# Performance work log

Hardware: AMD Instinct MI355X
Metric: run time of the kernel (lower is better)

The kernel has to match this reference:

```python
import jax, jax.numpy as jnp
import numpy as np

ALPHA = 0.1   # alpha_factor
BETA = 1.0    # beta_factor
NUM_CLASSES = 1000
B, D = 4096, 512


def setup_inputs() -> dict:
    key = jax.random.key(0)
    ks = jax.random.split(key, 7)
    return {
        "anchor": jax.random.normal(ks[0], (B, D), dtype=jnp.float32),
        "positive": jax.random.normal(ks[1], (B, D), dtype=jnp.float32),
        "negative": jax.random.normal(ks[2], (B, D), dtype=jnp.float32),
        "outputs": jax.random.normal(ks[3], (3 * B, NUM_CLASSES), dtype=jnp.float32),
        "labels_anchor": jax.random.randint(ks[4], (B,), 0, NUM_CLASSES, dtype=jnp.int32).astype(jnp.int64),
        "labels_neg": jax.random.randint(ks[5], (B,), 0, NUM_CLASSES, dtype=jnp.int32).astype(jnp.int64),
        "exemplars": jax.random.normal(ks[6], (NUM_CLASSES, D), dtype=jnp.float32),
    }


def reference(anchor, positive, negative, outputs, labels_anchor, labels_neg, exemplars):
    # cross-entropy (mean reduction) over concatenated labels [3B]
    labels = jnp.concatenate([labels_anchor, labels_anchor, labels_neg], axis=0)
    logp = jax.nn.log_softmax(outputs, axis=-1)                       # [3B, C]
    loss_softmax = -jnp.mean(jnp.take_along_axis(logp, labels[:, None], axis=1))

    # pairwise L2 distances anchor-to-exemplars via ||a||^2 + ||e||^2 - 2 a.e  -> [B, C]
    a_sq = jnp.sum(anchor * anchor, axis=1, keepdims=True)            # [B, 1]
    e_sq = jnp.sum(exemplars * exemplars, axis=1)[None, :]            # [1, C]
    d2 = a_sq + e_sq - 2.0 * (anchor @ exemplars.T)                   # [B, C]
    d_all = jnp.sqrt(jnp.maximum(d2, 0.0))

    d_ref = jnp.take_along_axis(d_all, labels_anchor[:, None], axis=1)[:, 0]  # [B]
    d_closest = jnp.min(d_all, axis=1)                                # [B]
    loss_center = jnp.sum(jax.nn.relu(d_ref - d_closest))

    tp = jnp.linalg.norm(anchor - positive, axis=1)                   # [B]
    tn = jnp.linalg.norm(anchor - negative, axis=1)                   # [B]
    loss_triplet = jnp.sum(jax.nn.relu(tp - tn))

    loss_total = loss_softmax + ALPHA * loss_center + BETA * loss_triplet
    return (loss_total, loss_triplet, loss_softmax, loss_center)
```

## Files before the change

### kernel.cpp

```cpp
#include <hip/hip_runtime.h>
#include <math.h>

#define BB 4096
#define DD 512
#define CC 1000

typedef __attribute__((ext_vector_type(8))) short short8;
typedef __attribute__((ext_vector_type(4))) float f32x4;

#define OFF_ABF  0
#define OFF_EBF  1048576
#define OFF_ESQ  1310720
#define OFF_ASQ  1311744
#define OFF_DREF 1315840
#define OFF_PMIN 1319936
#define OFF_CEP  1324032
#define OFF_TRP  1327104

__device__ __forceinline__ unsigned short f2bf(float x) {
    unsigned u = __float_as_uint(x);
    unsigned r = (u + 0x7FFFu + ((u >> 16) & 1u)) >> 16;
    return (unsigned short)r;
}

__global__ __launch_bounds__(256) void prep_kernel(
    const float* __restrict__ a, const float* __restrict__ p,
    const float* __restrict__ n, const float* __restrict__ ex,
    const int* __restrict__ la,
    unsigned short* __restrict__ Abf, unsigned short* __restrict__ Ebf,
    float* __restrict__ esq, float* __restrict__ asq,
    float* __restrict__ dref, float* __restrict__ tr_part,
    float* __restrict__ pmin)
{
    const int bid = blockIdx.x;
    const int wid = threadIdx.x >> 6, lane = threadIdx.x & 63;
    if (bid < 1024) {
        const int i = bid * 4 + wid;
        const int label = la[i];
        const float4* ar = (const float4*)(a + (size_t)i * DD);
        const float4* pr = (const float4*)(p + (size_t)i * DD);
        const float4* nr = (const float4*)(n + (size_t)i * DD);
        const float4* er = (const float4*)(ex + (size_t)label * DD);
        float sa = 0.f, sp = 0.f, sn = 0.f, se = 0.f;
#pragma unroll
        for (int k = 0; k < 2; k++) {
            const int j = lane + k * 64;
            float4 av = ar[j], pv = pr[j], nv = nr[j], ev = er[j];
            union { unsigned short u[4]; uint2 q; } o;
            o.u[0]=f2bf(av.x); o.u[1]=f2bf(av.y); o.u[2]=f2bf(av.z); o.u[3]=f2bf(av.w);
            *(uint2*)(Abf + (size_t)i * DD + j * 4) = o.q;
            sa += av.x*av.x + av.y*av.y + av.z*av.z + av.w*av.w;
            float dx = av.x-pv.x, dy = av.y-pv.y, dz = av.z-pv.z, dw = av.w-pv.w;
            sp += dx*dx + dy*dy + dz*dz + dw*dw;
            dx = av.x-nv.x; dy = av.y-nv.y; dz = av.z-nv.z; dw = av.w-nv.w;
            sn += dx*dx + dy*dy + dz*dz + dw*dw;
            dx = av.x-ev.x; dy = av.y-ev.y; dz = av.z-ev.z; dw = av.w-ev.w;
            se += dx*dx + dy*dy + dz*dz + dw*dw;
        }
        for (int off = 32; off; off >>= 1) {
            sa += __shfl_xor(sa, off);
            sp += __shfl_xor(sp, off);
            sn += __shfl_xor(sn, off);
            se += __shfl_xor(se, off);
        }
        __shared__ float ts[4];
        if (lane == 0) {
            asq[i]  = sa;
            dref[i] = sqrtf(se);
            pmin[i] = INFINITY;
            ts[wid] = fmaxf(sqrtf(sp) - sqrtf(sn), 0.f);
        }
        __syncthreads();
        if (threadIdx.x == 0) tr_part[bid] = ts[0] + ts[1] + ts[2] + ts[3];
    } else {
        const int c = (bid - 1024) * 4 + wid;
        float s = 0.f;
        if (c < CC) {
            const float4* row = (const float4*)(ex + (size_t)c * DD);
#pragma unroll
            for (int k = 0; k < 2; k++) {
                const int j = lane + k * 64;
                float4 v = row[j];
                union { unsigned short u[4]; uint2 q; } o;
                o.u[0]=f2bf(v.x); o.u[1]=f2bf(v.y); o.u[2]=f2bf(v.z); o.u[3]=f2bf(v.w);
                *(uint2*)(Ebf + (size_t)c * DD + j * 4) = o.q;
                s += v.x*v.x + v.y*v.y + v.z*v.z + v.w*v.w;
            }
            for (int off = 32; off; off >>= 1) s += __shfl_xor(s, off);
        } else {
            const uint2 z = make_uint2(0, 0);
#pragma unroll
            for (int k = 0; k < 2; k++) {
                const int j = lane + k * 64;
                *(uint2*)(Ebf + (size_t)c * DD + j * 4) = z;
            }
        }
        if (lane == 0) esq[c] = s;
    }
}

#define GL2LDS(gsrc, ldst) __builtin_amdgcn_global_load_lds( \
    (const __attribute__((address_space(1))) unsigned int*)(gsrc), \
    (__attribute__((address_space(3))) unsigned int*)(ldst), 16, 0, 0)

__global__ __launch_bounds__(512) void main_kernel(
    const unsigned short* __restrict__ Ab, const unsigned short* __restrict__ Eb,
    const float* __restrict__ asq, const float* __restrict__ esq,
    const float* __restrict__ outp,
    const int* __restrict__ la, const int* __restrict__ ln,
    float* __restrict__ pmin, float* __restrict__ ce_part)
{
    __shared__ unsigned short lA[2][256 * 32];
    __shared__ unsigned short lB[2][128 * 32];
    __shared__ float s_pm[2][256];
    __shared__ float ps[8];

    const int bid = blockIdx.x;
    const int tid = threadIdx.x;
    const int w = tid >> 6, lane = tid & 63;

    if (bid < 128) {
        const int wm = w >> 1, wn = w & 1;
        const int hi = lane >> 4, lo = lane & 15;
        const int gm0 = (bid >> 3) * 256, gn0 = (bid & 7) * 128;

        const int r0 = tid >> 2, q0 = tid & 3;
        const int sw0 = q0 ^ ((r0 >> 1) & 3);
        const size_t srcA0 = ((size_t)(gm0 + r0) << 9) + (sw0 << 3);
        const size_t srcA1 = ((size_t)(gm0 + 128 + r0) << 9) + (sw0 << 3);
        const size_t srcB  = ((size_t)(gn0 + r0) << 9) + (sw0 << 3);
        const int dstA = (w << 9);

#define STAGE(buf, kt) do { \
        GL2LDS(Ab + srcA0 + ((kt) << 5), &lA[buf][dstA]); \
        GL2LDS(Ab + srcA1 + ((kt) << 5), &lA[buf][4096 + dstA]); \
        GL2LDS(Eb + srcB  + ((kt) << 5), &lB[buf][dstA]); \
    } while (0)

        f32x4 acc[4][4];
#pragma unroll
        for (int mi = 0; mi < 4; mi++)
#pragma unroll
            for (int ni = 0; ni < 4; ni++) acc[mi][ni] = (f32x4){0.f, 0.f, 0.f, 0.f};

        STAGE(0, 0);
        for (int kt = 0; kt < 16; kt++) {
            const int buf = kt & 1;
            if (kt < 15) {
                STAGE(buf ^ 1, kt + 1);
                asm volatile("s_waitcnt vmcnt(3)" ::: "memory");
            } else {
                asm volatile("s_waitcnt vmcnt(0)" ::: "memory");
            }
            __builtin_amdgcn_s_barrier();
            asm volatile("" ::: "memory");

            short8 af[4], bf[4];
#pragma unroll
            for (int mi = 0; mi < 4; mi++) {
                int r = (wm << 6) + (mi << 4) + lo;
                af[mi] = *(const short8*)&lA[buf][(r << 5) + ((hi ^ ((r >> 1) & 3)) << 3)];
            }
#pragma unroll
            for (int ni = 0; ni < 4; ni++) {
                int r = (wn << 6) + (ni << 4) + lo;
                bf[ni] = *(const short8*)&lB[buf][(r << 5) + ((hi ^ ((r >> 1) & 3)) << 3)];
            }
#pragma unroll
            for (int mi = 0; mi < 4; mi++)
#pragma unroll
                for (int ni = 0; ni < 4; ni++)
                    acc[mi][ni] = __builtin_amdgcn_mfma_f32_16x16x32_bf16(af[mi], bf[ni], acc[mi][ni], 0, 0, 0);

            asm volatile("" ::: "memory");
            __builtin_amdgcn_s_barrier();
        }
#undef STAGE

        float aq[4][4];
#pragma unroll
        for (int mi = 0; mi < 4; mi++) {
            float4 a0 = *(const float4*)&asq[gm0 + wm * 64 + mi * 16 + hi * 4];
            aq[mi][0]=a0.x; aq[mi][1]=a0.y; aq[mi][2]=a0.z; aq[mi][3]=a0.w;
        }
        float esqc[4]; int bad[4];
#pragma unroll
        for (int ni = 0; ni < 4; ni++) {
            int gn = gn0 + wn * 64 + ni * 16 + lo;
            esqc[ni] = esq[gn];
            bad[ni] = (gn >= CC);
        }
        float vmin[4][4];
#pragma unroll
        for (int mi = 0; mi < 4; mi++)
#pragma unroll
            for (int j = 0; j < 4; j++) {
                float best = INFINITY;
#pragma unroll
                for (int ni = 0; ni < 4; ni++) {
                    float d2 = aq[mi][j] + esqc[ni] - 2.f * acc[mi][ni][j];
                    float d = sqrtf(fmaxf(d2, 0.f));
                    if (bad[ni]) d = INFINITY;
                    best = fminf(best, d);
                }
                vmin[mi][j] = best;
            }
#pragma unroll
        for (int off = 1; off < 16; off <<= 1)
#pragma unroll
            for (int mi = 0; mi < 4; mi++)
#pragma unroll
                for (int j = 0; j < 4; j++)
                    vmin[mi][j] = fminf(vmin[mi][j], __shfl_xor(vmin[mi][j], off));

        if (lo == 0) {
#pragma unroll
            for (int mi = 0; mi < 4; mi++)
#pragma unroll
                for (int j = 0; j < 4; j++)
                    s_pm[wn][wm * 64 + mi * 16 + hi * 4 + j] = vmin[mi][j];
        }
        __syncthreads();
        if (tid < 256) {
            float m2 = fminf(s_pm[0][tid], s_pm[1][tid]);
            atomicMin((int*)pmin + gm0 + tid, __float_as_int(m2));
        }
    } else {
        const int cb = bid - 128;
        const int r = cb * 8 + w;
        const int label = (r < 2 * BB) ? la[r & (BB - 1)] : ln[r - 2 * BB];
        const float4* row4 = (const float4*)(outp + (size_t)r * CC);
        float4 v[4];
#pragma unroll
        for (int k = 0; k < 4; k++) {
            int j4 = lane + k * 64;
            v[k] = (j4 < 250) ? row4[j4]
                              : make_float4(-INFINITY, -INFINITY, -INFINITY, -INFINITY);
        }
        float m = -INFINITY;
#pragma unroll
        for (int k = 0; k < 4; k++)
            m = fmaxf(m, fmaxf(fmaxf(v[k].x, v[k].y), fmaxf(v[k].z, v[k].w)));
        for (int off = 32; off; off >>= 1) m = fmaxf(m, __shfl_xor(m, off));

        const int lj4 = label >> 2, lc = label & 3;
        float s = 0.f, lv = 0.f;
#pragma unroll
        for (int k = 0; k < 4; k++) {
            int j4 = lane + k * 64;
            s += __expf(v[k].x - m) + __expf(v[k].y - m)
               + __expf(v[k].z - m) + __expf(v[k].w - m);
            float comp = (lc == 0) ? v[k].x : (lc == 1) ? v[k].y : (lc == 2) ? v[k].z : v[k].w;
            lv += (j4 == lj4) ? comp : 0.f;
        }
        for (int off = 32; off; off >>= 1) {
            s += __shfl_xor(s, off);
            lv += __shfl_xor(lv, off);
        }
        if (lane == 0) ps[w] = -(lv - m - __logf(s));
        __syncthreads();
        if (tid == 0) {
            float t = 0.f;
#pragma unroll
            for (int q = 0; q < 8; q++) t += ps[q];
            ce_part[cb] = t;
        }
    }
}

__global__ __launch_bounds__(1024) void final_kernel(
    const float* __restrict__ ce_part, const float* __restrict__ tr_part,
    const float* __restrict__ pmin, const float* __restrict__ dref,
    float* __restrict__ out)
{
    int tid = threadIdx.x;
    float ce = 0.f, tr = tr_part[tid], ctr = 0.f;
    if (tid < 1536) ce = ce_part[tid] + ((tid < 512) ? ce_part[tid + 1024] : 0.f);
#pragma unroll
    for (int a = 0; a < 4; a++) {
        int m = a * 1024 + tid;
        ctr += fmaxf(dref[m] - pmin[m], 0.f);
    }
    for (int off = 32; off; off >>= 1) {
        ce += __shfl_xor(ce, off);
        tr += __shfl_xor(tr, off);
        ctr += __shfl_xor(ctr, off);
    }
    __shared__ float s[3][16];
    int wid = tid >> 6, lane = tid & 63;
    if (lane == 0) { s[0][wid] = ce; s[1][wid] = tr; s[2][wid] = ctr; }
    __syncthreads();
    if (tid == 0) {
        float tce = 0.f, ttr = 0.f, tctr = 0.f;
#pragma unroll
        for (int w = 0; w < 16; w++) { tce += s[0][w]; ttr += s[1][w]; tctr += s[2][w]; }
        float lsm = tce / (3.f * BB);
        out[0] = lsm + 0.1f * tctr + 1.0f * ttr;
        out[1] = ttr;
        out[2] = lsm;
        out[3] = tctr;
    }
}

extern "C" void kernel_launch(void* const* d_in, const int* in_sizes, int n_in,
                              void* d_out, int out_size, void* d_ws, size_t ws_size,
                              hipStream_t stream) {
    const float* anchor   = (const float*)d_in[0];
    const float* positive = (const float*)d_in[1];
    const float* negative = (const float*)d_in[2];
    const float* outputs  = (const float*)d_in[3];
    const int*   la       = (const int*)d_in[4];
    const int*   ln       = (const int*)d_in[5];
    const float* ex       = (const float*)d_in[6];
    float* out = (float*)d_out;
    float* ws  = (float*)d_ws;

    unsigned short* Abf = (unsigned short*)(ws + OFF_ABF);
    unsigned short* Ebf = (unsigned short*)(ws + OFF_EBF);
    float* esq      = ws + OFF_ESQ;
    float* asq      = ws + OFF_ASQ;
    float* dref     = ws + OFF_DREF;
    float* pmin     = ws + OFF_PMIN;
    float* ce_part  = ws + OFF_CEP;
    float* tr_part  = ws + OFF_TRP;

    hipLaunchKernelGGL(prep_kernel,  dim3(1280), dim3(256),  0, stream,
                       anchor, positive, negative, ex, la, Abf, Ebf, esq, asq, dref, tr_part, pmin);
    hipLaunchKernelGGL(main_kernel,  dim3(1664), dim3(512),  0, stream,
                       Abf, Ebf, asq, esq, outputs, la, ln, pmin, ce_part);
    hipLaunchKernelGGL(final_kernel, dim3(1),    dim3(1024), 0, stream,
                       ce_part, tr_part, pmin, dref, out);
}
```

Baseline: 36.05 us.

## Move cross-entropy into prep kernel and run GEMM as its own small kernel

Moves the bandwidth-bound cross-entropy row processing out of the GEMM kernel and into the first kernel, alongside bf16 conversion and norm computation, using 512-thread blocks. The GEMM becomes a standalone 128-block kernel with a swapped tile index order (M-fastest). The aim is to overlap the large logits read with the prep work and to stop the GEMM blocks from sharing a launch with memory-bound CE blocks. The trade-off is that the GEMM now runs alone on only 128 blocks and can leave most CUs idle.

After: 38.08 us. 5.6% more time.

```diff
diff --git a/kernel.cpp b/kernel.cpp
--- a/kernel.cpp
+++ b/kernel.cpp
@@ -23,19 +23,62 @@
     return (unsigned short)r;
 }
 
-__global__ __launch_bounds__(256) void prep_kernel(
+__global__ __launch_bounds__(512) void k1_kernel(
     const float* __restrict__ a, const float* __restrict__ p,
     const float* __restrict__ n, const float* __restrict__ ex,
-    const int* __restrict__ la,
+    const float* __restrict__ outp,
+    const int* __restrict__ la, const int* __restrict__ ln,
     unsigned short* __restrict__ Abf, unsigned short* __restrict__ Ebf,
     float* __restrict__ esq, float* __restrict__ asq,
     float* __restrict__ dref, float* __restrict__ tr_part,
-    float* __restrict__ pmin)
+    float* __restrict__ pmin, float* __restrict__ ce_part)
 {
+    __shared__ float ps[8];
     const int bid = blockIdx.x;
-    const int wid = threadIdx.x >> 6, lane = threadIdx.x & 63;
-    if (bid < 1024) {
-        const int i = bid * 4 + wid;
+    const int tid = threadIdx.x;
+    const int w = tid >> 6, lane = tid & 63;
+
+    if (bid < 1536) {
+        const int r = bid * 8 + w;
+        const int label = (r < 2 * BB) ? la[r & (BB - 1)] : ln[r - 2 * BB];
+        const float4* row4 = (const float4*)(outp + (size_t)r * CC);
+        float4 v[4];
+#pragma unroll
+        for (int k = 0; k < 4; k++) {
+            int j4 = lane + k * 64;
+            v[k] = (j4 < 250) ? row4[j4]
+                              : make_float4(-INFINITY, -INFINITY, -INFINITY, -INFINITY);
+        }
+        float m = -INFINITY;
+#pragma unroll
+        for (int k = 0; k < 4; k++)
+            m = fmaxf(m, fmaxf(fmaxf(v[k].x, v[k].y), fmaxf(v[k].z, v[k].w)));
+        for (int off = 32; off; off >>= 1) m = fmaxf(m, __shfl_xor(m, off));
+
+        const int lj4 = label >> 2, lc = label & 3;
+        float s = 0.f, lv = 0.f;
+#pragma unroll
+        for (int k = 0; k < 4; k++) {
+            int j4 = lane + k * 64;
+            s += __expf(v[k].x - m) + __expf(v[k].y - m)
+               + __expf(v[k].z - m) + __expf(v[k].w - m);
+            float comp = (lc == 0) ? v[k].x : (lc == 1) ? v[k].y : (lc == 2) ? v[k].z : v[k].w;
+            lv += (j4 == lj4) ? comp : 0.f;
+        }
+        for (int off = 32; off; off >>= 1) {
+            s += __shfl_xor(s, off);
+            lv += __shfl_xor(lv, off);
+        }
+        if (lane == 0) ps[w] = -(lv - m - __logf(s));
+        __syncthreads();
+        if (tid == 0) {
+            float t = 0.f;
+#pragma unroll
+            for (int q = 0; q < 8; q++) t += ps[q];
+            ce_part[bid] = t;
+        }
+    } else if (bid < 2048) {
+        const int i = (bid - 1536) * 8 + w;
         const int label = la[i];
         const float4* ar = (const float4*)(a + (size_t)i * DD);
         const float4* pr = (const float4*)(p + (size_t)i * DD);
@@ -63,17 +106,21 @@
             sn += __shfl_xor(sn, off);
             se += __shfl_xor(se, off);
         }
-        __shared__ float ts[4];
         if (lane == 0) {
             asq[i]  = sa;
             dref[i] = sqrtf(se);
             pmin[i] = INFINITY;
-            ts[wid] = fmaxf(sqrtf(sp) - sqrtf(sn), 0.f);
+            ps[w] = fmaxf(sqrtf(sp) - sqrtf(sn), 0.f);
         }
         __syncthreads();
-        if (threadIdx.x == 0) tr_part[bid] = ts[0] + ts[1] + ts[2] + ts[3];
+        if (tid == 0) {
+            float t = 0.f;
+#pragma unroll
+            for (int q = 0; q < 8; q++) t += ps[q];
+            tr_part[bid - 1536] = t;
+        }
     } else {
-        const int c = (bid - 1024) * 4 + wid;
+        const int c = (bid - 2048) * 8 + w;
         float s = 0.f;
         if (c < CC) {
             const float4* row = (const float4*)(ex + (size_t)c * DD);
@@ -103,168 +150,123 @@
     (const __attribute__((address_space(1))) unsigned int*)(gsrc), \
     (__attribute__((address_space(3))) unsigned int*)(ldst), 16, 0, 0)
 
-__global__ __launch_bounds__(512) void main_kernel(
+__global__ __launch_bounds__(512) void gemm_kernel(
     const unsigned short* __restrict__ Ab, const unsigned short* __restrict__ Eb,
     const float* __restrict__ asq, const float* __restrict__ esq,
-    const float* __restrict__ outp,
-    const int* __restrict__ la, const int* __restrict__ ln,
-    float* __restrict__ pmin, float* __restrict__ ce_part)
+    float* __restrict__ pmin)
 {
     __shared__ unsigned short lA[2][256 * 32];
     __shared__ unsigned short lB[2][128 * 32];
     __shared__ float s_pm[2][256];
-    __shared__ float ps[8];
 
     const int bid = blockIdx.x;
     const int tid = threadIdx.x;
     const int w = tid >> 6, lane = tid & 63;
 
-    if (bid < 128) {
-        const int wm = w >> 1, wn = w & 1;
-        const int hi = lane >> 4, lo = lane & 15;
-        const int gm0 = (bid >> 3) * 256, gn0 = (bid & 7) * 128;
-
-        const int r0 = tid >> 2, q0 = tid & 3;
-        const int sw0 = q0 ^ ((r0 >> 1) & 3);
-        const size_t srcA0 = ((size_t)(gm0 + r0) << 9) + (sw0 << 3);
-        const size_t srcA1 = ((size_t)(gm0 + 128 + r0) << 9) + (sw0 << 3);
-        const size_t srcB  = ((size_t)(gn0 + r0) << 9) + (sw0 << 3);
-        const int dstA = (w << 9);
+    const int wm = w >> 1, wn = w & 1;
+    const int hi = lane >> 4, lo = lane & 15;
+    const int gm0 = (bid & 15) * 256, gn0 = (bid >> 4) * 128;
+
+    const int r0 = tid >> 2, q0 = tid & 3;
+    const int sw0 = q0 ^ ((r0 >> 1) & 3);
+    const size_t srcA0 = ((size_t)(gm0 + r0) << 9) + (sw0 << 3);
+    const size_t srcA1 = ((size_t)(gm0 + 128 + r0) << 9) + (sw0 << 3);
+    const size_t srcB  = ((size_t)(gn0 + r0) << 9) + (sw0 << 3);
+    const int dstA = (w << 9);
 
 #define STAGE(buf, kt) do { \
-        GL2LDS(Ab + srcA0 + ((kt) << 5), &lA[buf][dstA]); \
-        GL2LDS(Ab + srcA1 + ((kt) << 5), &lA[buf][4096 + dstA]); \
-        GL2LDS(Eb + srcB  + ((kt) << 5), &lB[buf][dstA]); \
-    } while (0)
-
-        f32x4 acc[4][4];
+    GL2LDS(Ab + srcA0 + ((kt) << 5), &lA[buf][dstA]); \
+    GL2LDS(Ab + srcA1 + ((kt) << 5), &lA[buf][4096 + dstA]); \
+    GL2LDS(Eb + srcB  + ((kt) << 5), &lB[buf][dstA]); \
+} while (0)
+
+    f32x4 acc[4][4];
+#pragma unroll
+    for (int mi = 0; mi < 4; mi++)
+#pragma unroll
+        for (int ni = 0; ni < 4; ni++) acc[mi][ni] = (f32x4){0.f, 0.f, 0.f, 0.f};
+
+    STAGE(0, 0);
+    for (int kt = 0; kt < 16; kt++) {
+        const int buf = kt & 1;
+        if (kt < 15) {
+            STAGE(buf ^ 1, kt + 1);
+            asm volatile("s_waitcnt vmcnt(3)" ::: "memory");
+        } else {
+            asm volatile("s_waitcnt vmcnt(0)" ::: "memory");
+        }
+        __builtin_amdgcn_s_barrier();
+        asm volatile("" ::: "memory");
+
+        short8 af[4], bf[4];
+#pragma unroll
+        for (int mi = 0; mi < 4; mi++) {
+            int r = (wm << 6) + (mi << 4) + lo;
+            af[mi] = *(const short8*)&lA[buf][(r << 5) + ((hi ^ ((r >> 1) & 3)) << 3)];
+        }
+#pragma unroll
+        for (int ni = 0; ni < 4; ni++) {
+            int r = (wn << 6) + (ni << 4) + lo;
+            bf[ni] = *(const short8*)&lB[buf][(r << 5) + ((hi ^ ((r >> 1) & 3)) << 3)];
+        }
 #pragma unroll
         for (int mi = 0; mi < 4; mi++)
 #pragma unroll
-            for (int ni = 0; ni < 4; ni++) acc[mi][ni] = (f32x4){0.f, 0.f, 0.f, 0.f};
-
-        STAGE(0, 0);
-        for (int kt = 0; kt < 16; kt++) {
-            const int buf = kt & 1;
-            if (kt < 15) {
-                STAGE(buf ^ 1, kt + 1);
-                asm volatile("s_waitcnt vmcnt(3)" ::: "memory");
-            } else {
-                asm volatile("s_waitcnt vmcnt(0)" ::: "memory");
+            for (int ni = 0; ni < 4; ni++)
+                acc[mi][ni] = __builtin_amdgcn_mfma_f32_16x16x32_bf16(af[mi], bf[ni], acc[mi][ni], 0, 0, 0);
+
+        asm volatile("" ::: "memory");
+        __builtin_amdgcn_s_barrier();
+    }
+#undef STAGE
+
+    float aq[4][4];
+#pragma unroll
+    for (int mi = 0; mi < 4; mi++) {
+        float4 a0 = *(const float4*)&asq[gm0 + wm * 64 + mi * 16 + hi * 4];
+        aq[mi][0]=a0.x; aq[mi][1]=a0.y; aq[mi][2]=a0.z; aq[mi][3]=a0.w;
+    }
+    float esqc[4]; int bad[4];
+#pragma unroll
+    for (int ni = 0; ni < 4; ni++) {
+        int gn = gn0 + wn * 64 + ni * 16 + lo;
+        esqc[ni] = esq[gn];
+        bad[ni] = (gn >= CC);
+    }
+    float vmin[4][4];
+#pragma unroll
+    for (int mi = 0; mi < 4; mi++)
+#pragma unroll
+        for (int j = 0; j < 4; j++) {
+            float best = INFINITY;
+#pragma unroll
+            for (int ni = 0; ni < 4; ni++) {
+                float d2 = aq[mi][j] + esqc[ni] - 2.f * acc[mi][ni][j];
+                float d = sqrtf(fmaxf(d2, 0.f));
+                if (bad[ni]) d = INFINITY;
+                best = fminf(best, d);
             }
-            __builtin_amdgcn_s_barrier();
-            asm volatile("" ::: "memory");
-
-            short8 af[4], bf[4];
-#pragma unroll
-            for (int mi = 0; mi < 4; mi++) {
-                int r = (wm << 6) + (mi << 4) + lo;
-                af[mi] = *(const short8*)&lA[buf][(r << 5) + ((hi ^ ((r >> 1) & 3)) << 3)];
-            }
-#pragma unroll
-            for (int ni = 0; ni < 4; ni++) {
-                int r = (wn << 6) + (ni << 4) + lo;
-                bf[ni] = *(const short8*)&lB[buf][(r << 5) + ((hi ^ ((r >> 1) & 3)) << 3)];
-            }
-#pragma unroll
-            for (int mi = 0; mi < 4; mi++)
-#pragma unroll
-                for (int ni = 0; ni < 4; ni++)
-                    acc[mi][ni] = __builtin_amdgcn_mfma_f32_16x16x32_bf16(af[mi], bf[ni], acc[mi][ni], 0, 0, 0);
-
-            asm volatile("" ::: "memory");
-            __builtin_amdgcn_s_barrier();
-        }
-#undef STAGE
-
-        float aq[4][4];
-#pragma unroll
-        for (int mi = 0; mi < 4; mi++) {
-            float4 a0 = *(const float4*)&asq[gm0 + wm * 64 + mi * 16 + hi * 4];
-            aq[mi][0]=a0.x; aq[mi][1]=a0.y; aq[mi][2]=a0.z; aq[mi][3]=a0.w;
-        }
-        float esqc[4]; int bad[4];
-#pragma unroll
-        for (int ni = 0; ni < 4; ni++) {
-            int gn = gn0 + wn * 64 + ni * 16 + lo;
-            esqc[ni] = esq[gn];
-            bad[ni] = (gn >= CC);
-        }
-        float vmin[4][4];
+            vmin[mi][j] = best;
+        }
+#pragma unroll
+    for (int off = 1; off < 16; off <<= 1)
 #pragma unroll
         for (int mi = 0; mi < 4; mi++)
 #pragma unroll
-            for (int j = 0; j < 4; j++) {
-                float best = INFINITY;
-#pragma unroll
-                for (int ni = 0; ni < 4; ni++) {
-                    float d2 = aq[mi][j] + esqc[ni] - 2.f * acc[mi][ni][j];
-                    float d = sqrtf(fmaxf(d2, 0.f));
-                    if (bad[ni]) d = INFINITY;
-                    best = fminf(best, d);
-                }
-                vmin[mi][j] = best;
-            }
-#pragma unroll
-        for (int off = 1; off < 16; off <<= 1)
-#pragma unroll
-            for (int mi = 0; mi < 4; mi++)
-#pragma unroll
-                for (int j = 0; j < 4; j++)
-                    vmin[mi][j] = fminf(vmin[mi][j], __shfl_xor(vmin[mi][j], off));
-
-        if (lo == 0) {
-#pragma unroll
-            for (int mi = 0; mi < 4; mi++)
-#pragma unroll
-                for (int j = 0; j < 4; j++)
-                    s_pm[wn][wm * 64 + mi * 16 + hi * 4 + j] = vmin[mi][j];
-        }
-        __syncthreads();
-        if (tid < 256) {
-            float m2 = fminf(s_pm[0][tid], s_pm[1][tid]);
-            atomicMin((int*)pmin + gm0 + tid, __float_as_int(m2));
-        }
-    } else {
-        const int cb = bid - 128;
-        const int r = cb * 8 + w;
-        const int label = (r < 2 * BB) ? la[r & (BB - 1)] : ln[r - 2 * BB];
-        const float4* row4 = (const float4*)(outp + (size_t)r * CC);
-        float4 v[4];
-#pragma unroll
-        for (int k = 0; k < 4; k++) {
-            int j4 = lane + k * 64;
-            v[k] = (j4 < 250) ? row4[j4]
-                              : make_float4(-INFINITY, -INFINITY, -INFINITY, -INFINITY);
-        }
-        float m = -INFINITY;
-#pragma unroll
-        for (int k = 0; k < 4; k++)
-            m = fmaxf(m, fmaxf(fmaxf(v[k].x, v[k].y), fmaxf(v[k].z, v[k].w)));
-        for (int off = 32; off; off >>= 1) m = fmaxf(m, __shfl_xor(m, off));
-
-        const int lj4 = label >> 2, lc = label & 3;
-        float s = 0.f, lv = 0.f;
-#pragma unroll
-        for (int k = 0; k < 4; k++) {
-            int j4 = lane + k * 64;
-            s += __expf(v[k].x - m) + __expf(v[k].y - m)
-               + __expf(v[k].z - m) + __expf(v[k].w - m);
-            float comp = (lc == 0) ? v[k].x : (lc == 1) ? v[k].y : (lc == 2) ? v[k].z : v[k].w;
-            lv += (j4 == lj4) ? comp : 0.f;
-        }
-        for (int off = 32; off; off >>= 1) {
-            s += __shfl_xor(s, off);
-            lv += __shfl_xor(lv, off);
-        }
-        if (lane == 0) ps[w] = -(lv - m - __logf(s));
-        __syncthreads();
-        if (tid == 0) {
-            float t = 0.f;
-#pragma unroll
-            for (int q = 0; q < 8; q++) t += ps[q];
-            ce_part[cb] = t;
-        }
+            for (int j = 0; j < 4; j++)
+                vmin[mi][j] = fminf(vmin[mi][j], __shfl_xor(vmin[mi][j], off));
+
+    if (lo == 0) {
+#pragma unroll
+        for (int mi = 0; mi < 4; mi++)
+#pragma unroll
+            for (int j = 0; j < 4; j++)
+                s_pm[wn][wm * 64 + mi * 16 + hi * 4 + j] = vmin[mi][j];
+    }
+    __syncthreads();
+    if (tid < 256) {
+        float m2 = fminf(s_pm[0][tid], s_pm[1][tid]);
+        atomicMin((int*)pmin + gm0 + tid, __float_as_int(m2));
     }
 }
 
@@ -274,7 +276,7 @@
     float* __restrict__ out)
 {
     int tid = threadIdx.x;
-    float ce = 0.f, tr = tr_part[tid], ctr = 0.f;
+    float ce = 0.f, tr = (tid < 512) ? tr_part[tid] : 0.f, ctr = 0.f;
     if (tid < 1536) ce = ce_part[tid] + ((tid < 512) ? ce_part[tid + 1024] : 0.f);
 #pragma unroll
     for (int a = 0; a < 4; a++) {
@@ -324,10 +326,11 @@
     float* ce_part  = ws + OFF_CEP;
     float* tr_part  = ws + OFF_TRP;
 
-    hipLaunchKernelGGL(prep_kernel,  dim3(1280), dim3(256),  0, stream,
-                       anchor, positive, negative, ex, la, Abf, Ebf, esq, asq, dref, tr_part, pmin);
-    hipLaunchKernelGGL(main_kernel,  dim3(1664), dim3(512),  0, stream,
-                       Abf, Ebf, asq, esq, outputs, la, ln, pmin, ce_part);
+    hipLaunchKernelGGL(k1_kernel,    dim3(2176), dim3(512),  0, stream,
+                       anchor, positive, negative, ex, outputs, la, ln,
+                       Abf, Ebf, esq, asq, dref, tr_part, pmin, ce_part);
+    hipLaunchKernelGGL(gemm_kernel,  dim3(128),  dim3(512),  0, stream,
+                       Abf, Ebf, asq, esq, pmin);
     hipLaunchKernelGGL(final_kernel, dim3(1),    dim3(1024), 0, stream,
                        ce_part, tr_part, pmin, dref, out);
 }
```
